# Kernel optimization log

Hardware: AMD Instinct MI355X
Metric: run time of the kernel (lower is better)

The kernel has to match this reference:

```python
import jax, jax.numpy as jnp
import numpy as np

T, B, I, H, FC, C = 256, 256, 1024, 256, 128, 8  # seq, batch, input, hidden, fc1, classes


def setup_inputs() -> dict:
    key = jax.random.key(0)
    ks = jax.random.split(key, 9)
    s_ih = 1.0 / np.sqrt(H)
    return {
        "x": jax.random.normal(ks[0], (T, B, I), dtype=jnp.float32),
        "W_ih": jax.random.uniform(ks[1], (4 * H, I), jnp.float32, -s_ih, s_ih),
        "W_hh": jax.random.uniform(ks[2], (4 * H, H), jnp.float32, -s_ih, s_ih),
        "b_ih": jax.random.uniform(ks[3], (4 * H,), jnp.float32, -s_ih, s_ih),
        "b_hh": jax.random.uniform(ks[4], (4 * H,), jnp.float32, -s_ih, s_ih),
        "W1": jax.random.uniform(ks[5], (FC, H), jnp.float32, -s_ih, s_ih),
        "b1": jax.random.uniform(ks[6], (FC,), jnp.float32, -s_ih, s_ih),
        "W2": jax.random.uniform(ks[7], (C, FC), jnp.float32, -1.0 / np.sqrt(FC), 1.0 / np.sqrt(FC)),
        "b2": jax.random.uniform(ks[8], (C,), jnp.float32, -1.0 / np.sqrt(FC), 1.0 / np.sqrt(FC)),
    }


def _lstm(x, W_ih, W_hh, b_ih, b_hh):
    # x: [T, B, I]; PyTorch gate order: i, f, g, o
    xg = jnp.einsum("tbi,gi->tbg", x, W_ih) + b_ih + b_hh  # precompute input projections [T,B,4H]

    def step(carry, xg_t):
        h, c = carry
        z = xg_t + h @ W_hh.T  # [B, 4H]
        i, f, g, o = jnp.split(z, 4, axis=-1)
        i = jax.nn.sigmoid(i)
        f = jax.nn.sigmoid(f)
        g = jnp.tanh(g)
        o = jax.nn.sigmoid(o)
        c = f * c + i * g
        h = o * jnp.tanh(c)
        return (h, c), h

    h0 = jnp.zeros((x.shape[1], W_hh.shape[1]), x.dtype)
    (hn, cn), out = jax.lax.scan(step, (h0, h0), xg)
    return out  # [T, B, H]


def reference(x, W_ih, W_hh, b_ih, b_hh, W1, b1, W2, b2):
    out = _lstm(x, W_ih, W_hh, b_ih, b_hh)      # [T, B, H]
    out = jax.nn.relu(out)
    out = jax.nn.relu(out @ W1.T + b1)           # [T, B, 128]
    out = out @ W2.T + b2                        # [T, B, num_classes]
    return out
```

## Files before the change

kernel.cpp:

```cpp
#include <hip/hip_runtime.h>
#include <type_traits>


typedef float    f4    __attribute__((ext_vector_type(4)));
typedef float    f32x4 __attribute__((ext_vector_type(4)));
typedef _Float16 h8    __attribute__((ext_vector_type(8)));
typedef _Float16 h4    __attribute__((ext_vector_type(4)));

__device__ __forceinline__ float ldf(const float* p)    { return *p; }
__device__ __forceinline__ float ldf(const _Float16* p) { return (float)*p; }

__device__ __forceinline__ float fast_sigmoid(float x) {
    return 1.f / (1.f + __expf(-x));
}
__device__ __forceinline__ float fast_tanh(float x) {
    const float e = __expf(-2.f * fabsf(x));
    const float t = (1.f - e) / (1.f + e);
    return copysignf(t, x);
}

__global__ __launch_bounds__(256) void k_bias(const float* __restrict__ b_ih,
                                              const float* __restrict__ b_hh,
                                              float* __restrict__ bias) {
    const int i = blockIdx.x * 256 + threadIdx.x;
    if (i < 1024) bias[i] = b_ih[i] + b_hh[i];
}

__global__ __launch_bounds__(256) void k_pack(const float* __restrict__ W_hh,
                                              _Float16* __restrict__ Wp) {
    const int idx = blockIdx.x * 256 + threadIdx.x;
    const int fi = idx >> 6;
    const int l  = idx & 63;
    const int g  = (fi >> 3) * 16 + (l & 15);
    const int k  = (fi & 7) * 32 + ((l >> 4) << 3);
    const float* src = &W_hh[(size_t)g * 256 + k];
    h8 v;
    #pragma unroll
    for (int c = 0; c < 8; ++c) v[c] = (_Float16)src[c];
    *(h8*)&Wp[(size_t)idx * 8] = v;
}

__global__ __launch_bounds__(256) void k_xg_mfma(
    const float* __restrict__ x, const float* __restrict__ W_ih,
    const float* __restrict__ bias, _Float16* __restrict__ xg2)
{
    __shared__ _Float16 As[2][128][40];
    __shared__ _Float16 Bs[2][128][40];
    const int tid = threadIdx.x;
    const int l   = tid & 63;
    const int w   = tid >> 6;
    const int m0  = blockIdx.y * 128;
    const int n0  = blockIdx.x * 128;
    const int wr  = (w >> 1) * 64;
    const int wc  = (w & 1) * 64;
    const int srow = tid >> 2;
    const int skof = (tid & 3) * 8;
    const int lr = l & 15;
    const int lg = l >> 4;

    f32x4 acc[4][4] = {};
    f4 ldA[2][2], ldB[2][2];

    auto XG_LOAD = [&](int kt) {
        const int k0 = kt * 32;
        #pragma unroll
        for (int s = 0; s < 2; ++s) {
            const float* xa = &x[(size_t)(m0 + srow + s * 64) * 1024 + k0 + skof];
            const float* wb = &W_ih[(size_t)(n0 + srow + s * 64) * 1024 + k0 + skof];
            ldA[s][0] = *(const f4*)xa; ldA[s][1] = *(const f4*)(xa + 4);
            ldB[s][0] = *(const f4*)wb; ldB[s][1] = *(const f4*)(wb + 4);
        }
    };
    auto XG_WRITE = [&](int buf) {
        #pragma unroll
        for (int s = 0; s < 2; ++s) {
            h8 va, vb;
            #pragma unroll
            for (int c = 0; c < 8; ++c) {
                va[c] = (_Float16)ldA[s][c >> 2][c & 3];
                vb[c] = (_Float16)ldB[s][c >> 2][c & 3];
            }
            *(h8*)&As[buf][srow + s * 64][skof] = va;
            *(h8*)&Bs[buf][srow + s * 64][skof] = vb;
        }
    };

    XG_LOAD(0);
    XG_WRITE(0);
    __syncthreads();
    for (int kt = 0; kt < 32; ++kt) {
        const int cur = kt & 1;
        if (kt + 1 < 32) XG_LOAD(kt + 1);
        h8 af[4], bf[4];
        #pragma unroll
        for (int mf = 0; mf < 4; ++mf) af[mf] = *(const h8*)&As[cur][wr + mf * 16 + lr][lg * 8];
        #pragma unroll
        for (int nf = 0; nf < 4; ++nf) bf[nf] = *(const h8*)&Bs[cur][wc + nf * 16 + lr][lg * 8];
        #pragma unroll
        for (int mf = 0; mf < 4; ++mf)
            #pragma unroll
            for (int nf = 0; nf < 4; ++nf)
                acc[mf][nf] = __builtin_amdgcn_mfma_f32_16x16x32_f16(af[mf], bf[nf], acc[mf][nf], 0, 0, 0);
        if (kt + 1 < 32) XG_WRITE((kt + 1) & 1);
        __syncthreads();
    }
    #pragma unroll
    for (int nf = 0; nf < 4; ++nf) {
        const int col  = n0 + wc + nf * 16 + lr;
        const float bv = bias[col];
        const int gate = col >> 8;
        const int w8   = (col >> 5) & 7;
        const int jt   = (col >> 4) & 1;
        #pragma unroll
        for (int mf = 0; mf < 4; ++mf) {
            const int rowb = m0 + wr + mf * 16 + lg * 4;
            const int tt = rowb >> 8;
            const int gb = (rowb >> 4) & 15;
            h4 pk;
            #pragma unroll
            for (int r = 0; r < 4; ++r) pk[r] = (_Float16)(acc[mf][nf][r] + bv);
            *(h4*)&xg2[((((size_t)tt * 16 + gb) * 8 + w8) * 64 + l) * 32 + gate * 8 + jt * 4] = pk;
        }
    }
}

__global__ __launch_bounds__(512, 2) void k_lstm_8w(
    const _Float16* __restrict__ xg2, const _Float16* __restrict__ Wp,
    _Float16* __restrict__ h_all)
{
    __shared__ _Float16 wlds[8 * 17 * 512];
    __shared__ _Float16 h_sh[2][16][264];
    const int tid = threadIdx.x;
    const int w  = tid >> 6;
    const int l  = tid & 63;
    const int lr = l & 15;
    const int lg = l >> 4;
    const int g  = blockIdx.x;
    const int b0 = g * 16;

    auto fgid = [&](int ti, int kb) {
        return (((ti >> 1) * 16 + w * 2 + (ti & 1)) * 8 + kb);
    };
    auto ldfrag = [&](int ti, int kb) {
        return *(const h8*)&Wp[((size_t)fgid(ti, kb) * 64 + l) * 8];
    };

    h8 wvg[24];
    #pragma unroll
    for (int kb = 0; kb < 3; ++kb)
        #pragma unroll
        for (int ti = 0; ti < 8; ++ti)
            wvg[kb * 8 + ti] = ldfrag(ti, kb);

    #pragma unroll
    for (int ti = 0; ti < 8; ++ti)
        *(h8*)&wlds[((w * 17 + ti) * 64 + l) * 8] = ldfrag(ti, 3);
    #pragma unroll
    for (int ti = 0; ti < 8; ++ti)
        *(h8*)&wlds[((w * 17 + 8 + ti) * 64 + l) * 8] = ldfrag(ti, 4);
    *(h8*)&wlds[((w * 17 + 16) * 64 + l) * 8] = ldfrag(0, 5);

    {
        _Float16* p = &h_sh[0][0][0];
        for (int i = tid; i < 2 * 16 * 264; i += 512) p[i] = (_Float16)0.f;
    }
    __syncthreads();

    float c[8];
    #pragma unroll
    for (int i = 0; i < 8; ++i) c[i] = 0.f;

    for (int t = 0; t < 256; ++t) {
        const int cur = t & 1;
        const int nxt = cur ^ 1;

        const size_t E = ((((size_t)t * 16 + g) * 8 + w) * 64 + l) * 32;
        h8 xq[4];
        #pragma unroll
        for (int q = 0; q < 4; ++q) xq[q] = *(const h8*)&xg2[E + q * 8];

        unsigned soff = 0;
        asm volatile("" : "+v"(soff));
        h8 sv[23];
        #pragma unroll
        for (int ti = 1; ti < 8; ++ti)
            sv[ti - 1] = *(const h8*)&Wp[((size_t)fgid(ti, 5) * 64 + l) * 8 + soff];
        #pragma unroll
        for (int ti = 0; ti < 8; ++ti)
            sv[7 + ti] = *(const h8*)&Wp[((size_t)fgid(ti, 6) * 64 + l) * 8 + soff];
        #pragma unroll
        for (int ti = 0; ti < 8; ++ti)
            sv[15 + ti] = *(const h8*)&Wp[((size_t)fgid(ti, 7) * 64 + l) * 8 + soff];

        f32x4 acc[8];
        #pragma unroll
        for (int ti = 0; ti < 8; ++ti) {
            #pragma unroll
            for (int r = 0; r < 4; ++r)
                acc[ti][r] = (float)xq[ti >> 1][(ti & 1) * 4 + r];
        }

        #pragma unroll
        for (int kb = 0; kb < 8; ++kb) {
            const h8 av = *(const h8*)&h_sh[cur][lr][kb * 32 + lg * 8];
            #pragma unroll
            for (int ti = 0; ti < 8; ++ti) {
                h8 b;
                if (kb < 3)                  b = wvg[kb * 8 + ti];
                else if (kb == 3)            b = *(const h8*)&wlds[((w * 17 + ti) * 64 + l) * 8];
                else if (kb == 4)            b = *(const h8*)&wlds[((w * 17 + 8 + ti) * 64 + l) * 8];
                else if (kb == 5 && ti == 0) b = *(const h8*)&wlds[((w * 17 + 16) * 64 + l) * 8];
                else if (kb == 5)            b = sv[ti - 1];
                else if (kb == 6)            b = sv[7 + ti];
                else                         b = sv[15 + ti];
                acc[ti] = __builtin_amdgcn_mfma_f32_16x16x32_f16(av, b, acc[ti], 0, 0, 0);
            }
        }

        #pragma unroll
        for (int jt = 0; jt < 2; ++jt) {
            #pragma unroll
            for (int r = 0; r < 4; ++r) {
                const float ig = fast_sigmoid(acc[0 * 2 + jt][r]);
                const float fg = fast_sigmoid(acc[1 * 2 + jt][r]);
                const float gg = fast_tanh(acc[2 * 2 + jt][r]);
                const float og = fast_sigmoid(acc[3 * 2 + jt][r]);
                const int ci = jt * 4 + r;
                c[ci] = fg * c[ci] + ig * gg;
                const float hv = og * fast_tanh(c[ci]);
                const _Float16 h16 = (_Float16)hv;
                h_sh[nxt][lg * 4 + r][w * 32 + jt * 16 + lr] = h16;
                h_all[((size_t)t * 256 + b0 + lg * 4 + r) * 256 + w * 32 + jt * 16 + lr] = h16;
            }
        }
        __syncthreads();
    }
}

template <typename HT>
__global__ __launch_bounds__(256) void k_fc(
    const HT* __restrict__ h_all, const float* __restrict__ W1,
    const float* __restrict__ b1, const float* __restrict__ W2,
    const float* __restrict__ b2, float* __restrict__ out)
{
    __shared__ __align__(16) float smem[12288];
    float* hsT = smem;
    float* w1T = smem + 4096;
    const int tid = threadIdx.x;
    const int m0 = blockIdx.x * 64;
    const int tx = tid & 15;
    const int ty = tid >> 4;
    const int r0 = ty * 4;
    const int fA = tx * 4;
    const int fB = 64 + tx * 4;
    float acc[4][8] = {};
    for (int kc = 0; kc < 4; ++kc) {
        const int k0 = kc * 64;
        __syncthreads();
        #pragma unroll
        for (int i = 0; i < 4; ++i) {
            const int fid = tid + i * 256;
            const int rr = fid >> 4;
            const int qq = fid & 15;
            const HT* p = &h_all[(size_t)(m0 + rr) * 256 + k0 + qq * 4];
            f4 v;
            if constexpr (std::is_same<HT, float>::value) {
                v = *(const f4*)p;
            } else {
                v[0] = ldf(p); v[1] = ldf(p + 1); v[2] = ldf(p + 2); v[3] = ldf(p + 3);
            }
            #pragma unroll
            for (int cc = 0; cc < 4; ++cc)
                hsT[(qq * 4 + cc) * 64 + rr] = fmaxf(v[cc], 0.f);
        }
        #pragma unroll
        for (int i = 0; i < 8; ++i) {
            const int fid = tid + i * 256;
            const int ff = fid >> 4;
            const int qq = fid & 15;
            const f4 v = *(const f4*)&W1[(size_t)ff * 256 + k0 + qq * 4];
            #pragma unroll
            for (int cc = 0; cc < 4; ++cc)
                w1T[(qq * 4 + cc) * 128 + ff] = v[cc];
        }
        __syncthreads();
        #pragma unroll 4
        for (int kk = 0; kk < 64; ++kk) {
            const f4 aa = *(const f4*)&hsT[kk * 64 + r0];
            const f4 ba = *(const f4*)&w1T[kk * 128 + fA];
            const f4 bb = *(const f4*)&w1T[kk * 128 + fB];
            #pragma unroll
            for (int i = 0; i < 4; ++i) {
                #pragma unroll
                for (int j = 0; j < 4; ++j) {
                    acc[i][j]     = fmaf(aa[i], ba[j], acc[i][j]);
                    acc[i][j + 4] = fmaf(aa[i], bb[j], acc[i][j + 4]);
                }
            }
        }
    }
    __syncthreads();
    float* fc1s = smem;
    #pragma unroll
    for (int j = 0; j < 4; ++j) {
        const float bbA = b1[fA + j];
        const float bbB = b1[fB + j];
        #pragma unroll
        for (int i = 0; i < 4; ++i) {
            fc1s[(r0 + i) * 132 + fA + j] = fmaxf(acc[i][j] + bbA, 0.f);
            fc1s[(r0 + i) * 132 + fB + j] = fmaxf(acc[i][j + 4] + bbB, 0.f);
        }
    }
    __syncthreads();
    const int r  = tid >> 2;
    const int c0 = (tid & 3) * 2;
    float o0 = b2[c0], o1 = b2[c0 + 1];
    #pragma unroll
    for (int fq = 0; fq < 32; ++fq) {
        const f4 p  = *(const f4*)&fc1s[r * 132 + fq * 4];
        const f4 wa = *(const f4*)&W2[(size_t)c0 * 128 + fq * 4];
        const f4 wb = *(const f4*)&W2[(size_t)(c0 + 1) * 128 + fq * 4];
        o0 += p[0] * wa[0] + p[1] * wa[1] + p[2] * wa[2] + p[3] * wa[3];
        o1 += p[0] * wb[0] + p[1] * wb[1] + p[2] * wb[2] + p[3] * wb[3];
    }
    out[(size_t)(m0 + r) * 8 + c0]     = o0;
    out[(size_t)(m0 + r) * 8 + c0 + 1] = o1;
}

extern "C" void kernel_launch(void* const* d_in, const int* in_sizes, int n_in,
                              void* d_out, int out_size, void* d_ws, size_t ws_size,
                              hipStream_t stream)
{
    const float* x    = (const float*)d_in[0];
    const float* W_ih = (const float*)d_in[1];
    const float* W_hh = (const float*)d_in[2];
    const float* b_ih = (const float*)d_in[3];
    const float* b_hh = (const float*)d_in[4];
    const float* W1   = (const float*)d_in[5];
    const float* b1   = (const float*)d_in[6];
    const float* W2   = (const float*)d_in[7];
    const float* b2   = (const float*)d_in[8];
    float* out = (float*)d_out;
    char* ws = (char*)d_ws;

    _Float16* xg2   = (_Float16*)ws;
    _Float16* h_all = (_Float16*)(ws + 134217728);
    _Float16* Wp    = (_Float16*)(ws + 167772160);
    float*    bias  = (float*)   (ws + 168296448);

    k_bias<<<4, 256, 0, stream>>>(b_ih, b_hh, bias);
    k_pack<<<128, 256, 0, stream>>>(W_hh, Wp);
    k_xg_mfma<<<dim3(8, 512), 256, 0, stream>>>(x, W_ih, bias, xg2);
    k_lstm_8w<<<16, 512, 0, stream>>>(xg2, Wp, h_all);
    k_fc<_Float16><<<1024, 256, 0, stream>>>(h_all, W1, b1, W2, b2, out);
}
```

Baseline: 1.996 ms.

## Restage LSTM recurrent weights and prefetch next-step input projections

The recurrent kernel now keeps two k-blocks of W_hh in registers (loaded via inline asm to pin them) instead of three. It shifts the LDS-resident blocks down by one and streams the remaining four k-blocks from global memory in three staggered groups interleaved with the MFMA chains. The next timestep's input-projection values are prefetched during the current step. The full __syncthreads is replaced by an explicit lgkmcnt wait, s_barrier and sched_barrier. The aim is to hide global-load latency on the serial recurrence and cut register pressure, at the cost of more global traffic per step and reliance on hand-placed waits for correctness.

New measurement: 2.029 ms. About the same (+1.6%).

```diff
diff --git a/kernel.cpp b/kernel.cpp
--- a/kernel.cpp
+++ b/kernel.cpp
@@ -17,6 +17,14 @@
     const float e = __expf(-2.f * fabsf(x));
     const float t = (1.f - e) / (1.f + e);
     return copysignf(t, x);
+}
+
+__device__ __forceinline__ f32x4 ld_pin(const _Float16* p) {
+    f32x4 d;
+    asm volatile("global_load_dwordx4 %0, %1, off\n\t"
+                 "s_waitcnt vmcnt(0)"
+                 : "=v"(d) : "v"(p) : "memory");
+    return d;
 }
 
 __global__ __launch_bounds__(256) void k_bias(const float* __restrict__ b_ih,
@@ -145,20 +153,20 @@
         return *(const h8*)&Wp[((size_t)fgid(ti, kb) * 64 + l) * 8];
     };
 
-    h8 wvg[24];
-    #pragma unroll
-    for (int kb = 0; kb < 3; ++kb)
+    f32x4 wpin[16];
+    #pragma unroll
+    for (int kb = 0; kb < 2; ++kb)
         #pragma unroll
         for (int ti = 0; ti < 8; ++ti)
-            wvg[kb * 8 + ti] = ldfrag(ti, kb);
+            wpin[kb * 8 + ti] = ld_pin(&Wp[((size_t)fgid(ti, kb) * 64 + l) * 8]);
 
     #pragma unroll
     for (int ti = 0; ti < 8; ++ti)
-        *(h8*)&wlds[((w * 17 + ti) * 64 + l) * 8] = ldfrag(ti, 3);
+        *(h8*)&wlds[((w * 17 + ti) * 64 + l) * 8] = ldfrag(ti, 2);
     #pragma unroll
     for (int ti = 0; ti < 8; ++ti)
-        *(h8*)&wlds[((w * 17 + 8 + ti) * 64 + l) * 8] = ldfrag(ti, 4);
-    *(h8*)&wlds[((w * 17 + 16) * 64 + l) * 8] = ldfrag(0, 5);
+        *(h8*)&wlds[((w * 17 + 8 + ti) * 64 + l) * 8] = ldfrag(ti, 3);
+    *(h8*)&wlds[((w * 17 + 16) * 64 + l) * 8] = ldfrag(0, 4);
 
     {
         _Float16* p = &h_sh[0][0][0];
@@ -170,28 +178,17 @@
     #pragma unroll
     for (int i = 0; i < 8; ++i) c[i] = 0.f;
 
+    h8 xq[4];
+    {
+        const size_t E0 = (((size_t)g * 8 + w) * 64 + l) * 32;
+        #pragma unroll
+        for (int q = 0; q < 4; ++q) xq[q] = *(const h8*)&xg2[E0 + q * 8];
+    }
+
     for (int t = 0; t < 256; ++t) {
         const int cur = t & 1;
         const int nxt = cur ^ 1;
 
-        const size_t E = ((((size_t)t * 16 + g) * 8 + w) * 64 + l) * 32;
-        h8 xq[4];
-        #pragma unroll
-        for (int q = 0; q < 4; ++q) xq[q] = *(const h8*)&xg2[E + q * 8];
-
-        unsigned soff = 0;
-        asm volatile("" : "+v"(soff));
-        h8 sv[23];
-        #pragma unroll
-        for (int ti = 1; ti < 8; ++ti)
-            sv[ti - 1] = *(const h8*)&Wp[((size_t)fgid(ti, 5) * 64 + l) * 8 + soff];
-        #pragma unroll
-        for (int ti = 0; ti < 8; ++ti)
-            sv[7 + ti] = *(const h8*)&Wp[((size_t)fgid(ti, 6) * 64 + l) * 8 + soff];
-        #pragma unroll
-        for (int ti = 0; ti < 8; ++ti)
-            sv[15 + ti] = *(const h8*)&Wp[((size_t)fgid(ti, 7) * 64 + l) * 8 + soff];
-
         f32x4 acc[8];
         #pragma unroll
         for (int ti = 0; ti < 8; ++ti) {
@@ -200,21 +197,87 @@
                 acc[ti][r] = (float)xq[ti >> 1][(ti & 1) * 4 + r];
         }
 
-        #pragma unroll
-        for (int kb = 0; kb < 8; ++kb) {
-            const h8 av = *(const h8*)&h_sh[cur][lr][kb * 32 + lg * 8];
+        h8 xqn[4];
+        if (t < 255) {
+            const size_t En = ((((size_t)(t + 1) * 16 + g) * 8 + w) * 64 + l) * 32;
+            #pragma unroll
+            for (int q = 0; q < 4; ++q) xqn[q] = *(const h8*)&xg2[En + q * 8];
+        }
+
+        unsigned sA = 0;
+        asm volatile("" : "+v"(sA));
+        h8 sv4[7], sv5[8];
+        #pragma unroll
+        for (int ti = 1; ti < 8; ++ti)
+            sv4[ti - 1] = *(const h8*)&Wp[((size_t)fgid(ti, 4) * 64 + l) * 8 + sA];
+        #pragma unroll
+        for (int ti = 0; ti < 8; ++ti)
+            sv5[ti] = *(const h8*)&Wp[((size_t)fgid(ti, 5) * 64 + l) * 8 + sA];
+
+        {
+            h8 av = *(const h8*)&h_sh[cur][lr][0 * 32 + lg * 8];
+            #pragma unroll
+            for (int ti = 0; ti < 8; ++ti)
+                acc[ti] = __builtin_amdgcn_mfma_f32_16x16x32_f16(av, __builtin_bit_cast(h8, wpin[ti]), acc[ti], 0, 0, 0);
+            av = *(const h8*)&h_sh[cur][lr][1 * 32 + lg * 8];
+            #pragma unroll
+            for (int ti = 0; ti < 8; ++ti)
+                acc[ti] = __builtin_amdgcn_mfma_f32_16x16x32_f16(av, __builtin_bit_cast(h8, wpin[8 + ti]), acc[ti], 0, 0, 0);
+        }
+
+        unsigned sB = 0;
+        asm volatile("" : "+v"(sB));
+        h8 sv6[8];
+        #pragma unroll
+        for (int ti = 0; ti < 8; ++ti)
+            sv6[ti] = *(const h8*)&Wp[((size_t)fgid(ti, 6) * 64 + l) * 8 + sB];
+
+        {
+            h8 av = *(const h8*)&h_sh[cur][lr][2 * 32 + lg * 8];
             #pragma unroll
             for (int ti = 0; ti < 8; ++ti) {
-                h8 b;
-                if (kb < 3)                  b = wvg[kb * 8 + ti];
-                else if (kb == 3)            b = *(const h8*)&wlds[((w * 17 + ti) * 64 + l) * 8];
-                else if (kb == 4)            b = *(const h8*)&wlds[((w * 17 + 8 + ti) * 64 + l) * 8];
-                else if (kb == 5 && ti == 0) b = *(const h8*)&wlds[((w * 17 + 16) * 64 + l) * 8];
-                else if (kb == 5)            b = sv[ti - 1];
-                else if (kb == 6)            b = sv[7 + ti];
-                else                         b = sv[15 + ti];
+                const h8 b = *(const h8*)&wlds[((w * 17 + ti) * 64 + l) * 8];
                 acc[ti] = __builtin_amdgcn_mfma_f32_16x16x32_f16(av, b, acc[ti], 0, 0, 0);
             }
+            av = *(const h8*)&h_sh[cur][lr][3 * 32 + lg * 8];
+            #pragma unroll
+            for (int ti = 0; ti < 8; ++ti) {
+                const h8 b = *(const h8*)&wlds[((w * 17 + 8 + ti) * 64 + l) * 8];
+                acc[ti] = __builtin_amdgcn_mfma_f32_16x16x32_f16(av, b, acc[ti], 0, 0, 0);
+            }
+        }
+
+        {
+            h8 av = *(const h8*)&h_sh[cur][lr][4 * 32 + lg * 8];
+            {
+                const h8 b = *(const h8*)&wlds[((w * 17 + 16) * 64 + l) * 8];
+                acc[0] = __builtin_amdgcn_mfma_f32_16x16x32_f16(av, b, acc[0], 0, 0, 0);
+            }
+            #pragma unroll
+            for (int ti = 1; ti < 8; ++ti)
+                acc[ti] = __builtin_amdgcn_mfma_f32_16x16x32_f16(av, sv4[ti - 1], acc[ti], 0, 0, 0);
+            av = *(const h8*)&h_sh[cur][lr][5 * 32 + lg * 8];
+            #pragma unroll
+            for (int ti = 0; ti < 8; ++ti)
+                acc[ti] = __builtin_amdgcn_mfma_f32_16x16x32_f16(av, sv5[ti], acc[ti], 0, 0, 0);
+        }
+
+        unsigned sC = 0;
+        asm volatile("" : "+v"(sC));
+        h8 sv7[8];
+        #pragma unroll
+        for (int ti = 0; ti < 8; ++ti)
+            sv7[ti] = *(const h8*)&Wp[((size_t)fgid(ti, 7) * 64 + l) * 8 + sC];
+
+        {
+            h8 av = *(const h8*)&h_sh[cur][lr][6 * 32 + lg * 8];
+            #pragma unroll
+            for (int ti = 0; ti < 8; ++ti)
+                acc[ti] = __builtin_amdgcn_mfma_f32_16x16x32_f16(av, sv6[ti], acc[ti], 0, 0, 0);
+            av = *(const h8*)&h_sh[cur][lr][7 * 32 + lg * 8];
+            #pragma unroll
+            for (int ti = 0; ti < 8; ++ti)
+                acc[ti] = __builtin_amdgcn_mfma_f32_16x16x32_f16(av, sv7[ti], acc[ti], 0, 0, 0);
         }
 
         #pragma unroll
@@ -233,7 +296,15 @@
                 h_all[((size_t)t * 256 + b0 + lg * 4 + r) * 256 + w * 32 + jt * 16 + lr] = h16;
             }
         }
-        __syncthreads();
+
+        if (t < 255) {
+            #pragma unroll
+            for (int q = 0; q < 4; ++q) xq[q] = xqn[q];
+        }
+
+        asm volatile("s_waitcnt lgkmcnt(0)" ::: "memory");
+        __builtin_amdgcn_s_barrier();
+        __builtin_amdgcn_sched_barrier(0);
     }
 }
 
```

## Restructure LSTM recurrence into 8 blocks of 16 waves, two batch groups each

Applied to the files above, without the earlier changes.

The recurrent kernel now launches 8 workgroups of 1024 threads instead of 16 of 512. Each wave owns 16 hidden columns across all four gates for two 16-row batch groups, so every W_hh fragment feeds two MFMAs. W_hh fragments not kept in LDS are streamed from global memory with double-buffered prefetch. The xg layout is rewritten to match, the bias add is folded into the projection kernel, and tanh uses a cheaper formula. The change trades fewer parallel blocks and a larger barrier scope for better weight reuse and less weight traffic per step.

Result: slower. 2.644 ms (+32.4%).

```diff
diff --git a/kernel.cpp b/kernel.cpp
--- a/kernel.cpp
+++ b/kernel.cpp
@@ -14,16 +14,7 @@
     return 1.f / (1.f + __expf(-x));
 }
 __device__ __forceinline__ float fast_tanh(float x) {
-    const float e = __expf(-2.f * fabsf(x));
-    const float t = (1.f - e) / (1.f + e);
-    return copysignf(t, x);
-}
-
-__global__ __launch_bounds__(256) void k_bias(const float* __restrict__ b_ih,
-                                              const float* __restrict__ b_hh,
-                                              float* __restrict__ bias) {
-    const int i = blockIdx.x * 256 + threadIdx.x;
-    if (i < 1024) bias[i] = b_ih[i] + b_hh[i];
+    return 1.f - 2.f / (1.f + __expf(2.f * x));
 }
 
 __global__ __launch_bounds__(256) void k_pack(const float* __restrict__ W_hh,
@@ -42,7 +33,8 @@
 
 __global__ __launch_bounds__(256) void k_xg_mfma(
     const float* __restrict__ x, const float* __restrict__ W_ih,
-    const float* __restrict__ bias, _Float16* __restrict__ xg2)
+    const float* __restrict__ b_ih, const float* __restrict__ b_hh,
+    _Float16* __restrict__ xg2)
 {
     __shared__ _Float16 As[2][128][40];
     __shared__ _Float16 Bs[2][128][40];
@@ -107,133 +99,161 @@
     #pragma unroll
     for (int nf = 0; nf < 4; ++nf) {
         const int col  = n0 + wc + nf * 16 + lr;
-        const float bv = bias[col];
+        const float bv = b_ih[col] + b_hh[col];
         const int gate = col >> 8;
-        const int w8   = (col >> 5) & 7;
-        const int jt   = (col >> 4) & 1;
+        const int w16  = (col >> 4) & 15;
         #pragma unroll
         for (int mf = 0; mf < 4; ++mf) {
             const int rowb = m0 + wr + mf * 16 + lg * 4;
             const int tt = rowb >> 8;
-            const int gb = (rowb >> 4) & 15;
+            const int b  = rowb & 255;
+            const int g8 = b >> 5;
+            const int G  = (b >> 4) & 1;
             h4 pk;
             #pragma unroll
             for (int r = 0; r < 4; ++r) pk[r] = (_Float16)(acc[mf][nf][r] + bv);
-            *(h4*)&xg2[((((size_t)tt * 16 + gb) * 8 + w8) * 64 + l) * 32 + gate * 8 + jt * 4] = pk;
-        }
-    }
-}
-
-__global__ __launch_bounds__(512, 2) void k_lstm_8w(
-    const _Float16* __restrict__ xg2, const _Float16* __restrict__ Wp,
-    _Float16* __restrict__ h_all)
+            *(h4*)&xg2[(((((size_t)tt * 8 + g8) * 2 + G) * 16 + w16) * 64 + l) * 16 + gate * 4] = pk;
+        }
+    }
+}
+
+__global__
+__attribute__((amdgpu_flat_work_group_size(1024, 1024), amdgpu_waves_per_eu(4, 4)))
+void k_lstm_2g(const _Float16* __restrict__ xg2, const _Float16* __restrict__ Wp,
+               _Float16* __restrict__ h_all)
 {
-    __shared__ _Float16 wlds[8 * 17 * 512];
-    __shared__ _Float16 h_sh[2][16][264];
+    __shared__ _Float16 wlds[16 * 7 * 512];
+    __shared__ _Float16 h_sh[2][2][16][270];
     const int tid = threadIdx.x;
     const int w  = tid >> 6;
     const int l  = tid & 63;
     const int lr = l & 15;
     const int lg = l >> 4;
     const int g  = blockIdx.x;
-    const int b0 = g * 16;
-
-    auto fgid = [&](int ti, int kb) {
-        return (((ti >> 1) * 16 + w * 2 + (ti & 1)) * 8 + kb);
+    const int b0 = g * 32;
+
+    auto fgid = [&](int gate, int kb) { return (gate * 16 + w) * 8 + kb; };
+    auto ldfrag = [&](int gate, int kb) {
+        return *(const h8*)&Wp[((size_t)fgid(gate, kb) * 64 + l) * 8];
     };
-    auto ldfrag = [&](int ti, int kb) {
-        return *(const h8*)&Wp[((size_t)fgid(ti, kb) * 64 + l) * 8];
-    };
-
-    h8 wvg[24];
-    #pragma unroll
-    for (int kb = 0; kb < 3; ++kb)
-        #pragma unroll
-        for (int ti = 0; ti < 8; ++ti)
-            wvg[kb * 8 + ti] = ldfrag(ti, kb);
-
-    #pragma unroll
-    for (int ti = 0; ti < 8; ++ti)
-        *(h8*)&wlds[((w * 17 + ti) * 64 + l) * 8] = ldfrag(ti, 3);
-    #pragma unroll
-    for (int ti = 0; ti < 8; ++ti)
-        *(h8*)&wlds[((w * 17 + 8 + ti) * 64 + l) * 8] = ldfrag(ti, 4);
-    *(h8*)&wlds[((w * 17 + 16) * 64 + l) * 8] = ldfrag(0, 5);
+
+    #pragma unroll
+    for (int gate = 0; gate < 4; ++gate)
+        *(h8*)&wlds[((w * 7 + gate) * 64 + l) * 8] = ldfrag(gate, 0);
+    #pragma unroll
+    for (int gate = 0; gate < 3; ++gate)
+        *(h8*)&wlds[((w * 7 + 4 + gate) * 64 + l) * 8] = ldfrag(gate, 1);
 
     {
-        _Float16* p = &h_sh[0][0][0];
-        for (int i = tid; i < 2 * 16 * 264; i += 512) p[i] = (_Float16)0.f;
+        _Float16* p = &h_sh[0][0][0][0];
+        for (int i = tid; i < 2 * 2 * 16 * 270; i += 1024) p[i] = (_Float16)0.f;
     }
     __syncthreads();
 
-    float c[8];
-    #pragma unroll
-    for (int i = 0; i < 8; ++i) c[i] = 0.f;
+    float c[2][4] = {};
 
     for (int t = 0; t < 256; ++t) {
         const int cur = t & 1;
         const int nxt = cur ^ 1;
 
-        const size_t E = ((((size_t)t * 16 + g) * 8 + w) * 64 + l) * 32;
-        h8 xq[4];
-        #pragma unroll
-        for (int q = 0; q < 4; ++q) xq[q] = *(const h8*)&xg2[E + q * 8];
+        const size_t E0 = ((((size_t)t * 8 + g) * 2 + 0) * 16 + w) * 64 * 16 + (size_t)l * 16;
+        const size_t E1 = E0 + (size_t)16 * 64 * 16;
+        h8 xa0 = *(const h8*)&xg2[E0];
+        h8 xa1 = *(const h8*)&xg2[E0 + 8];
+        h8 xb0 = *(const h8*)&xg2[E1];
+        h8 xb1 = *(const h8*)&xg2[E1 + 8];
+
+        f32x4 acc[2][4];
+        #pragma unroll
+        for (int gate = 0; gate < 4; ++gate) {
+            #pragma unroll
+            for (int r = 0; r < 4; ++r) {
+                const int v = gate * 4 + r;
+                acc[0][gate][r] = (float)((v < 8) ? xa0[v] : xa1[v - 8]);
+                acc[1][gate][r] = (float)((v < 8) ? xb0[v] : xb1[v - 8]);
+            }
+        }
 
         unsigned soff = 0;
         asm volatile("" : "+v"(soff));
-        h8 sv[23];
-        #pragma unroll
-        for (int ti = 1; ti < 8; ++ti)
-            sv[ti - 1] = *(const h8*)&Wp[((size_t)fgid(ti, 5) * 64 + l) * 8 + soff];
-        #pragma unroll
-        for (int ti = 0; ti < 8; ++ti)
-            sv[7 + ti] = *(const h8*)&Wp[((size_t)fgid(ti, 6) * 64 + l) * 8 + soff];
-        #pragma unroll
-        for (int ti = 0; ti < 8; ++ti)
-            sv[15 + ti] = *(const h8*)&Wp[((size_t)fgid(ti, 7) * 64 + l) * 8 + soff];
-
-        f32x4 acc[8];
-        #pragma unroll
-        for (int ti = 0; ti < 8; ++ti) {
-            #pragma unroll
-            for (int r = 0; r < 4; ++r)
-                acc[ti][r] = (float)xq[ti >> 1][(ti & 1) * 4 + r];
-        }
-
-        #pragma unroll
-        for (int kb = 0; kb < 8; ++kb) {
-            const h8 av = *(const h8*)&h_sh[cur][lr][kb * 32 + lg * 8];
-            #pragma unroll
-            for (int ti = 0; ti < 8; ++ti) {
-                h8 b;
-                if (kb < 3)                  b = wvg[kb * 8 + ti];
-                else if (kb == 3)            b = *(const h8*)&wlds[((w * 17 + ti) * 64 + l) * 8];
-                else if (kb == 4)            b = *(const h8*)&wlds[((w * 17 + 8 + ti) * 64 + l) * 8];
-                else if (kb == 5 && ti == 0) b = *(const h8*)&wlds[((w * 17 + 16) * 64 + l) * 8];
-                else if (kb == 5)            b = sv[ti - 1];
-                else if (kb == 6)            b = sv[7 + ti];
-                else                         b = sv[15 + ti];
-                acc[ti] = __builtin_amdgcn_mfma_f32_16x16x32_f16(av, b, acc[ti], 0, 0, 0);
-            }
-        }
-
-        #pragma unroll
-        for (int jt = 0; jt < 2; ++jt) {
+        auto ldstream = [&](int gate, int kb) {
+            return *(const h8*)&Wp[((size_t)fgid(gate, kb) * 64 + l) * 8 + soff];
+        };
+
+        h8 s1g3 = ldstream(3, 1);
+        h8 sv0[4], sv1[4];
+        #pragma unroll
+        for (int gate = 0; gate < 4; ++gate) sv0[gate] = ldstream(gate, 2);
+        #pragma unroll
+        for (int gate = 0; gate < 4; ++gate) sv1[gate] = ldstream(gate, 3);
+
+        {
+            const h8 a0 = *(const h8*)&h_sh[0][cur][lr][0 * 32 + lg * 8];
+            const h8 a1 = *(const h8*)&h_sh[1][cur][lr][0 * 32 + lg * 8];
+            #pragma unroll
+            for (int gate = 0; gate < 4; ++gate) {
+                const h8 b = *(const h8*)&wlds[((w * 7 + gate) * 64 + l) * 8];
+                acc[0][gate] = __builtin_amdgcn_mfma_f32_16x16x32_f16(a0, b, acc[0][gate], 0, 0, 0);
+                acc[1][gate] = __builtin_amdgcn_mfma_f32_16x16x32_f16(a1, b, acc[1][gate], 0, 0, 0);
+            }
+        }
+        {
+            const h8 a0 = *(const h8*)&h_sh[0][cur][lr][1 * 32 + lg * 8];
+            const h8 a1 = *(const h8*)&h_sh[1][cur][lr][1 * 32 + lg * 8];
+            #pragma unroll
+            for (int gate = 0; gate < 4; ++gate) {
+                const h8 b = (gate < 3) ? *(const h8*)&wlds[((w * 7 + 4 + gate) * 64 + l) * 8]
+                                        : s1g3;
+                acc[0][gate] = __builtin_amdgcn_mfma_f32_16x16x32_f16(a0, b, acc[0][gate], 0, 0, 0);
+                acc[1][gate] = __builtin_amdgcn_mfma_f32_16x16x32_f16(a1, b, acc[1][gate], 0, 0, 0);
+            }
+        }
+        #pragma unroll
+        for (int kb = 2; kb < 8; ++kb) {
+            const h8 a0 = *(const h8*)&h_sh[0][cur][lr][kb * 32 + lg * 8];
+            const h8 a1 = *(const h8*)&h_sh[1][cur][lr][kb * 32 + lg * 8];
+            if (kb & 1) {
+                #pragma unroll
+                for (int gate = 0; gate < 4; ++gate) {
+                    acc[0][gate] = __builtin_amdgcn_mfma_f32_16x16x32_f16(a0, sv1[gate], acc[0][gate], 0, 0, 0);
+                    acc[1][gate] = __builtin_amdgcn_mfma_f32_16x16x32_f16(a1, sv1[gate], acc[1][gate], 0, 0, 0);
+                }
+                if (kb + 2 < 8) {
+                    #pragma unroll
+                    for (int gate = 0; gate < 4; ++gate) sv1[gate] = ldstream(gate, kb + 2);
+                }
+            } else {
+                #pragma unroll
+                for (int gate = 0; gate < 4; ++gate) {
+                    acc[0][gate] = __builtin_amdgcn_mfma_f32_16x16x32_f16(a0, sv0[gate], acc[0][gate], 0, 0, 0);
+                    acc[1][gate] = __builtin_amdgcn_mfma_f32_16x16x32_f16(a1, sv0[gate], acc[1][gate], 0, 0, 0);
+                }
+                if (kb + 2 < 8) {
+                    #pragma unroll
+                    for (int gate = 0; gate < 4; ++gate) sv0[gate] = ldstream(gate, kb + 2);
+                }
+            }
+        }
+
+        #pragma unroll
+        for (int G = 0; G < 2; ++G) {
             #pragma unroll
             for (int r = 0; r < 4; ++r) {
-                const float ig = fast_sigmoid(acc[0 * 2 + jt][r]);
-                const float fg = fast_sigmoid(acc[1 * 2 + jt][r]);
-                const float gg = fast_tanh(acc[2 * 2 + jt][r]);
-                const float og = fast_sigmoid(acc[3 * 2 + jt][r]);
-                const int ci = jt * 4 + r;
-                c[ci] = fg * c[ci] + ig * gg;
-                const float hv = og * fast_tanh(c[ci]);
+                const float ig = fast_sigmoid(acc[G][0][r]);
+                const float fg = fast_sigmoid(acc[G][1][r]);
+                const float gg = fast_tanh(acc[G][2][r]);
+                const float og = fast_sigmoid(acc[G][3][r]);
+                c[G][r] = fg * c[G][r] + ig * gg;
+                const float hv = og * fast_tanh(c[G][r]);
                 const _Float16 h16 = (_Float16)hv;
-                h_sh[nxt][lg * 4 + r][w * 32 + jt * 16 + lr] = h16;
-                h_all[((size_t)t * 256 + b0 + lg * 4 + r) * 256 + w * 32 + jt * 16 + lr] = h16;
-            }
-        }
-        __syncthreads();
+                h_sh[G][nxt][lg * 4 + r][w * 16 + lr] = h16;
+                h_all[((size_t)t * 256 + b0 + G * 16 + lg * 4 + r) * 256 + w * 16 + lr] = h16;
+            }
+        }
+
+        asm volatile("s_waitcnt lgkmcnt(0)" ::: "memory");
+        __builtin_amdgcn_s_barrier();
+        __builtin_amdgcn_sched_barrier(0);
     }
 }
 
@@ -346,11 +366,9 @@
     _Float16* xg2   = (_Float16*)ws;
     _Float16* h_all = (_Float16*)(ws + 134217728);
     _Float16* Wp    = (_Float16*)(ws + 167772160);
-    float*    bias  = (float*)   (ws + 168296448);
-
-    k_bias<<<4, 256, 0, stream>>>(b_ih, b_hh, bias);
+
     k_pack<<<128, 256, 0, stream>>>(W_hh, Wp);
-    k_xg_mfma<<<dim3(8, 512), 256, 0, stream>>>(x, W_ih, bias, xg2);
-    k_lstm_8w<<<16, 512, 0, stream>>>(xg2, Wp, h_all);
+    k_xg_mfma<<<dim3(8, 512), 256, 0, stream>>>(x, W_ih, b_ih, b_hh, xg2);
+    k_lstm_2g<<<8, 1024, 0, stream>>>(xg2, Wp, h_all);
     k_fc<_Float16><<<1024, 256, 0, stream>>>(h_all, W1, b1, W2, b2, out);
 }
```

## Stream W_hh through double-buffered LDS window with async global-to-LDS loads

Applied to the files above, without the earlier changes.

The recurrent LSTM kernel no longer keeps part of W_hh resident in registers and LDS. Instead it streams every k-block of the packed weights each timestep into a two-slot LDS window using global_load_lds, with manual vmcnt waits so loads overlap the MFMAs. The next timestep's input projection is prefetched during the current step. The separate bias kernel is folded into the xg GEMM epilogue. This frees registers and LDS but re-reads the whole weight matrix from L2 every step, and the hand-written waitcnt accounting is fragile.

Result: slower. 2.086 ms (+4.5%).

```diff
diff --git a/kernel.cpp b/kernel.cpp
--- a/kernel.cpp
+++ b/kernel.cpp
@@ -19,11 +19,13 @@
     return copysignf(t, x);
 }
 
-__global__ __launch_bounds__(256) void k_bias(const float* __restrict__ b_ih,
-                                              const float* __restrict__ b_hh,
-                                              float* __restrict__ bias) {
-    const int i = blockIdx.x * 256 + threadIdx.x;
-    if (i < 1024) bias[i] = b_ih[i] + b_hh[i];
+#define WAITVM(n) do { asm volatile("s_waitcnt vmcnt(" #n ")" ::: "memory"); \
+                       __builtin_amdgcn_sched_barrier(0); } while (0)
+
+__device__ __forceinline__ void stage16(const _Float16* g, _Float16* l) {
+    __builtin_amdgcn_global_load_lds(
+        (const __attribute__((address_space(1))) void*)g,
+        (__attribute__((address_space(3))) void*)l, 16, 0, 0);
 }
 
 __global__ __launch_bounds__(256) void k_pack(const float* __restrict__ W_hh,
@@ -42,7 +44,8 @@
 
 __global__ __launch_bounds__(256) void k_xg_mfma(
     const float* __restrict__ x, const float* __restrict__ W_ih,
-    const float* __restrict__ bias, _Float16* __restrict__ xg2)
+    const float* __restrict__ b_ih, const float* __restrict__ b_hh,
+    _Float16* __restrict__ xg2)
 {
     __shared__ _Float16 As[2][128][40];
     __shared__ _Float16 Bs[2][128][40];
@@ -107,7 +110,7 @@
     #pragma unroll
     for (int nf = 0; nf < 4; ++nf) {
         const int col  = n0 + wc + nf * 16 + lr;
-        const float bv = bias[col];
+        const float bv = b_ih[col] + b_hh[col];
         const int gate = col >> 8;
         const int w8   = (col >> 5) & 7;
         const int jt   = (col >> 4) & 1;
@@ -124,11 +127,11 @@
     }
 }
 
-__global__ __launch_bounds__(512, 2) void k_lstm_8w(
+__global__ __launch_bounds__(512, 2) void k_lstm_st(
     const _Float16* __restrict__ xg2, const _Float16* __restrict__ Wp,
     _Float16* __restrict__ h_all)
 {
-    __shared__ _Float16 wlds[8 * 17 * 512];
+    __shared__ _Float16 wwin[8 * 2 * 8 * 512];
     __shared__ _Float16 h_sh[2][16][264];
     const int tid = threadIdx.x;
     const int w  = tid >> 6;
@@ -141,24 +144,12 @@
     auto fgid = [&](int ti, int kb) {
         return (((ti >> 1) * 16 + w * 2 + (ti & 1)) * 8 + kb);
     };
-    auto ldfrag = [&](int ti, int kb) {
-        return *(const h8*)&Wp[((size_t)fgid(ti, kb) * 64 + l) * 8];
+    auto STAGE = [&](int kb, int buf) {
+        #pragma unroll
+        for (int ti = 0; ti < 8; ++ti)
+            stage16(&Wp[((size_t)fgid(ti, kb) * 64 + l) * 8],
+                    &wwin[((w * 2 + buf) * 8 + ti) * 512]);
     };
-
-    h8 wvg[24];
-    #pragma unroll
-    for (int kb = 0; kb < 3; ++kb)
-        #pragma unroll
-        for (int ti = 0; ti < 8; ++ti)
-            wvg[kb * 8 + ti] = ldfrag(ti, kb);
-
-    #pragma unroll
-    for (int ti = 0; ti < 8; ++ti)
-        *(h8*)&wlds[((w * 17 + ti) * 64 + l) * 8] = ldfrag(ti, 3);
-    #pragma unroll
-    for (int ti = 0; ti < 8; ++ti)
-        *(h8*)&wlds[((w * 17 + 8 + ti) * 64 + l) * 8] = ldfrag(ti, 4);
-    *(h8*)&wlds[((w * 17 + 16) * 64 + l) * 8] = ldfrag(0, 5);
 
     {
         _Float16* p = &h_sh[0][0][0];
@@ -170,27 +161,20 @@
     #pragma unroll
     for (int i = 0; i < 8; ++i) c[i] = 0.f;
 
+    h8 xq[4];
+    {
+        const size_t E0 = (((size_t)g * 8 + w) * 64 + l) * 32;
+        #pragma unroll
+        for (int q = 0; q < 4; ++q) xq[q] = *(const h8*)&xg2[E0 + q * 8];
+    }
+    STAGE(0, 0);
+    STAGE(1, 1);
+
     for (int t = 0; t < 256; ++t) {
         const int cur = t & 1;
         const int nxt = cur ^ 1;
 
-        const size_t E = ((((size_t)t * 16 + g) * 8 + w) * 64 + l) * 32;
-        h8 xq[4];
-        #pragma unroll
-        for (int q = 0; q < 4; ++q) xq[q] = *(const h8*)&xg2[E + q * 8];
-
-        unsigned soff = 0;
-        asm volatile("" : "+v"(soff));
-        h8 sv[23];
-        #pragma unroll
-        for (int ti = 1; ti < 8; ++ti)
-            sv[ti - 1] = *(const h8*)&Wp[((size_t)fgid(ti, 5) * 64 + l) * 8 + soff];
-        #pragma unroll
-        for (int ti = 0; ti < 8; ++ti)
-            sv[7 + ti] = *(const h8*)&Wp[((size_t)fgid(ti, 6) * 64 + l) * 8 + soff];
-        #pragma unroll
-        for (int ti = 0; ti < 8; ++ti)
-            sv[15 + ti] = *(const h8*)&Wp[((size_t)fgid(ti, 7) * 64 + l) * 8 + soff];
+        WAITVM(16);
 
         f32x4 acc[8];
         #pragma unroll
@@ -201,20 +185,25 @@
         }
 
         #pragma unroll
-        for (int kb = 0; kb < 8; ++kb) {
-            const h8 av = *(const h8*)&h_sh[cur][lr][kb * 32 + lg * 8];
+        for (int cb = 0; cb < 8; ++cb) {
+            if (cb < 7) WAITVM(8); else WAITVM(0);
+            const h8 av = *(const h8*)&h_sh[cur][lr][cb * 32 + lg * 8];
             #pragma unroll
             for (int ti = 0; ti < 8; ++ti) {
-                h8 b;
-                if (kb < 3)                  b = wvg[kb * 8 + ti];
-                else if (kb == 3)            b = *(const h8*)&wlds[((w * 17 + ti) * 64 + l) * 8];
-                else if (kb == 4)            b = *(const h8*)&wlds[((w * 17 + 8 + ti) * 64 + l) * 8];
-                else if (kb == 5 && ti == 0) b = *(const h8*)&wlds[((w * 17 + 16) * 64 + l) * 8];
-                else if (kb == 5)            b = sv[ti - 1];
-                else if (kb == 6)            b = sv[7 + ti];
-                else                         b = sv[15 + ti];
+                const h8 b = *(const h8*)&wwin[((w * 2 + (cb & 1)) * 8 + ti) * 512 + l * 8];
                 acc[ti] = __builtin_amdgcn_mfma_f32_16x16x32_f16(av, b, acc[ti], 0, 0, 0);
             }
+            if (cb + 2 < 8) {
+                __builtin_amdgcn_sched_barrier(0);
+                STAGE(cb + 2, cb & 1);
+            }
+        }
+
+        h8 xqn[4];
+        if (t < 255) {
+            const size_t En = ((((size_t)(t + 1) * 16 + g) * 8 + w) * 64 + l) * 32;
+            #pragma unroll
+            for (int q = 0; q < 4; ++q) xqn[q] = *(const h8*)&xg2[En + q * 8];
         }
 
         #pragma unroll
@@ -233,7 +222,17 @@
                 h_all[((size_t)t * 256 + b0 + lg * 4 + r) * 256 + w * 32 + jt * 16 + lr] = h16;
             }
         }
-        __syncthreads();
+
+        if (t < 255) {
+            STAGE(0, 0);
+            STAGE(1, 1);
+            #pragma unroll
+            for (int q = 0; q < 4; ++q) xq[q] = xqn[q];
+        }
+
+        asm volatile("s_waitcnt lgkmcnt(0)" ::: "memory");
+        __builtin_amdgcn_s_barrier();
+        __builtin_amdgcn_sched_barrier(0);
     }
 }
 
@@ -346,11 +345,9 @@
     _Float16* xg2   = (_Float16*)ws;
     _Float16* h_all = (_Float16*)(ws + 134217728);
     _Float16* Wp    = (_Float16*)(ws + 167772160);
-    float*    bias  = (float*)   (ws + 168296448);
-
-    k_bias<<<4, 256, 0, stream>>>(b_ih, b_hh, bias);
+
     k_pack<<<128, 256, 0, stream>>>(W_hh, Wp);
-    k_xg_mfma<<<dim3(8, 512), 256, 0, stream>>>(x, W_ih, bias, xg2);
-    k_lstm_8w<<<16, 512, 0, stream>>>(xg2, Wp, h_all);
+    k_xg_mfma<<<dim3(8, 512), 256, 0, stream>>>(x, W_ih, b_ih, b_hh, xg2);
+    k_lstm_st<<<16, 512, 0, stream>>>(xg2, Wp, h_all);
     k_fc<_Float16><<<1024, 256, 0, stream>>>(h_all, W1, b1, W2, b2, out);
 }
```
